# Optimization experiments

Hardware: AMD Instinct MI355X
Metric: run time of the kernel (lower is better)

Reference implementation:

```python
import jax, jax.numpy as jnp
import numpy as np

B, T, E, H = 4, 2048, 1024, 2048  # note: T must equal H (mask shape constraint in source)


def setup_inputs() -> dict:
    key = jax.random.key(0)
    ks = jax.random.split(key, 5)
    x = jax.random.normal(ks[0], (B, T, E), dtype=jnp.float32)
    Wq = jax.random.normal(ks[1], (E, H), dtype=jnp.float32) * 0.02
    bq = jnp.zeros((H,), dtype=jnp.float32)
    Wv = jax.random.normal(ks[2], (E, H), dtype=jnp.float32) * 0.02
    bv = jnp.zeros((H,), dtype=jnp.float32)
    return {"x": x, "Wq": Wq, "bq": bq, "Wv": Wv, "bv": bv}


def reference(x, Wq, bq, Wv, bv):
    # NOTE: original code uses q_proj for BOTH q and k (k = self.q_proj(x)),
    # so k is identical to q; k_proj params are dead. We reproduce that.
    q = x @ Wq + bq                                  # [B, T, H]
    v = x @ Wv + bv                                  # [B, T, H]
    scores = jnp.einsum('bqd,bkd->bqk', q, q)        # q @ k.mT with k == q
    scaled = scores / jnp.sqrt(jnp.float32(Wq.shape[1]))
    mask = jnp.tril(jnp.ones((scaled.shape[1], scaled.shape[2]), dtype=scaled.dtype))
    masked = scaled * mask                           # multiplicative mask (as in source)
    attn = jax.nn.softmax(masked, axis=1)            # softmax over dim=1 (query axis), as in source
    return attn @ v                                  # [B, T, H]
```

## Files before the change

kernel.cpp:

```cpp
#include <hip/hip_runtime.h>


#define B_DIM 4
#define T_DIM 2048
#define E_DIM 1024
#define H_DIM 2048

typedef __attribute__((ext_vector_type(8))) short bf16x8;
typedef __attribute__((ext_vector_type(4))) short s16x4;
typedef __attribute__((ext_vector_type(4))) float f32x4;

__device__ __forceinline__ float bf2f(short s) {
  union { float f; unsigned u; } x; x.u = ((unsigned)(unsigned short)s) << 16; return x.f;
}
__device__ __forceinline__ short f2bf(float f) {
  union { float f; unsigned u; } x; x.f = f;
  unsigned r = x.u + 0x7fff + ((x.u >> 16) & 1);
  return (short)(r >> 16);
}

__device__ __forceinline__ void gload16(const short* g, short* l) {
  __builtin_amdgcn_global_load_lds(
      (const __attribute__((address_space(1))) void*)g,
      (__attribute__((address_space(3))) void*)l, 16, 0, 0);
}

__device__ __forceinline__ void bar() {
  __builtin_amdgcn_sched_barrier(0);
  __builtin_amdgcn_s_barrier();
  __builtin_amdgcn_sched_barrier(0);
}

__global__ __launch_bounds__(512, 2) void gemm_pv(
    const short* __restrict__ Pg, const short* __restrict__ Vg,
    float* __restrict__ Cg, const float* __restrict__ sfx)
{
  __shared__ __align__(16) short lds[24576];

  const int t = threadIdx.x;
  const int lane = t & 63, wave = t >> 6;
  const int wm = wave >> 2, wn = wave & 3;
  const int l16 = lane & 15, kg = lane >> 4;

  const int lin = blockIdx.x + 256 * blockIdx.y;
  const int rt = 15 - (lin >> 5);
  const int rem = lin & 31;
  const int ct = rem >> 2, bz = rem & 3;

  const int K = T_DIM, N = H_DIM;
  const short* A  = Pg + (long)bz * T_DIM * T_DIM + (long)rt * 128 * K;
  const short* Bv = Vg + (long)bz * H_DIM * T_DIM + (long)ct * 256 * K;
  const int NT = (rt + 1) * 2;

  const int fA = t >> 3, cA = (t & 7) ^ (fA & 7);
  const long sA0 = (long)(2 * fA + (cA >> 2)) * K + (cA & 3) * 8;
  const int dA0 = t * 8;
  long sB[2]; int dB[2];
#pragma unroll
  for (int j = 0; j < 2; ++j) {
    const int cid = j * 512 + t;
    const int f = cid >> 3, c = (cid & 7) ^ (f & 7);
    sB[j] = (long)(2 * f + (c >> 2)) * K + (c & 3) * 8;
    dB[j] = cid * 8;
  }

  const int fl = l16 >> 1;
  const int slot = (((l16 & 1) * 4 + kg) ^ fl) & 7;
  const int abase = (wm * 32 + fl) * 64 + slot * 8;
  const int bbase = 8192 + (wn * 32 + fl) * 64 + slot * 8;

  f32x4 acc[4][4] = {};

  for (int tt = 0; tt < NT; ++tt) {
    const long k0 = (long)tt * 64;
    __syncthreads();
    gload16(A  + sA0   + k0,      &lds[dA0]);
    gload16(A  + sA0   + k0 + 32, &lds[4096 + dA0]);
    gload16(Bv + sB[0] + k0,      &lds[8192 + dB[0]]);
    gload16(Bv + sB[1] + k0,      &lds[8192 + dB[1]]);
    gload16(Bv + sB[0] + k0 + 32, &lds[16384 + dB[0]]);
    gload16(Bv + sB[1] + k0 + 32, &lds[16384 + dB[1]]);
    __syncthreads();
#pragma unroll
    for (int kk = 0; kk < 2; ++kk) {
      bf16x8 bfr[4];
#pragma unroll
      for (int ni = 0; ni < 4; ++ni)
        bfr[ni] = *(const bf16x8*)&lds[bbase + kk * 8192 + ni * 512];
#pragma unroll
      for (int mi = 0; mi < 4; ++mi) {
        const bf16x8 a = *(const bf16x8*)&lds[abase + kk * 4096 + mi * 512];
#pragma unroll
        for (int ni = 0; ni < 4; ++ni)
          acc[mi][ni] = __builtin_amdgcn_mfma_f32_16x16x32_bf16(a, bfr[ni], acc[mi][ni], 0, 0, 0);
      }
    }
  }

  float* C = Cg + (long)bz * T_DIM * H_DIM;
  const float* sf = sfx + ((long)bz * 16 + rt) * N;
  const int rowb = rt * 128 + wm * 64 + kg * 4;
  const int colb = ct * 256 + wn * 64 + l16;
#pragma unroll
  for (int mi = 0; mi < 4; ++mi)
#pragma unroll
    for (int ni = 0; ni < 4; ++ni) {
      const int col = colb + ni * 16;
      const float s = sf[col];
#pragma unroll
      for (int r = 0; r < 4; ++r)
        C[(long)(rowb + mi * 16 + r) * N + col] = acc[mi][ni][r] + s;
    }
}

template<int MODE>
__global__ __launch_bounds__(512, 2) void gemm256(
    const short* __restrict__ Ag, const short* __restrict__ Bg,
    const float* __restrict__ bias, const float* __restrict__ bias2,
    void* __restrict__ Cg, void* __restrict__ Cg2,
    const float* __restrict__ sfx,
    int N, int K, long sA, long sB, long sC)
{
  __shared__ __align__(16) short lds[2 * 32768];

  const int t = threadIdx.x;
  const int lane = t & 63, wave = t >> 6;
  const int wm = wave >> 2, wn = wave & 3;
  const int l16 = lane & 15, kg = lane >> 4;

  int rt, ct, bz;
  {
    int lin = blockIdx.y * gridDim.x + blockIdx.x;
    const int cpx = (gridDim.x * gridDim.y) >> 3;
    lin = (lin & 7) * cpx + (lin >> 3);
    rt = lin / gridDim.x; ct = lin - rt * gridDim.x;
    bz = 0;
  }

  const short* A  = Ag + (long)bz * sA + (long)rt * 256 * K;
  const short* Bp = Bg + (long)bz * sB + (long)ct * 256 * K;
  const int kEnd = K;
  const int NT = kEnd >> 6;

  long soff[2];
  int dsto[2];
#pragma unroll
  for (int j = 0; j < 2; ++j) {
    const int cid = j * 512 + t;
    const int f = cid >> 3, sl = cid & 7;
    const int c = sl ^ (f & 7);
    soff[j] = (long)(2 * f + (c >> 2)) * K + (c & 3) * 8;
    dsto[j] = cid * 8;
  }

  const int fl = l16 >> 1;
  const int slot = (((l16 & 1) * 4 + kg) ^ fl) & 7;
  const int aoff = (wm * 64 + fl) * 64 + slot * 8;
  const int boff = (wn * 32 + fl) * 64 + slot * 8;

  f32x4 acc[8][4] = {};

  {
    short* S = lds;
#pragma unroll
    for (int kh = 0; kh < 2; ++kh)
#pragma unroll
      for (int j = 0; j < 2; ++j) {
        gload16(A  + soff[j] + kh * 32, &S[kh * 8192 + dsto[j]]);
        gload16(Bp + soff[j] + kh * 32, &S[16384 + kh * 8192 + dsto[j]]);
      }
  }
  asm volatile("s_waitcnt vmcnt(4)");
  __builtin_amdgcn_sched_barrier(0);
  bar();

  for (int T = 0; T < NT; ++T) {
    const short* Abase = lds + (T & 1) * 32768;
    short* S = lds + ((T + 1) & 1) * 32768;
    const long kIss = (long)(T + 1) * 64;
    const bool st = (T + 1) < NT;
    bf16x8 bfr[4], af[4];

    {
      const short* Ab = Abase;
      const short* Bb = Abase + 16384;
#pragma unroll
      for (int n = 0; n < 4; ++n) bfr[n] = *(const bf16x8*)&Bb[boff + n * 512];
#pragma unroll
      for (int m = 0; m < 4; ++m) af[m] = *(const bf16x8*)&Ab[aoff + m * 512];
      if (st) {
        gload16(A + soff[0] + kIss, &S[dsto[0]]);
        gload16(A + soff[1] + kIss, &S[dsto[1]]);
      }
      bar();
      __builtin_amdgcn_s_setprio(1);
#pragma unroll
      for (int m = 0; m < 4; ++m)
#pragma unroll
        for (int n = 0; n < 4; ++n)
          acc[m][n] = __builtin_amdgcn_mfma_f32_16x16x32_bf16(af[m], bfr[n], acc[m][n], 0, 0, 0);
      __builtin_amdgcn_s_setprio(0);
      bar();
    }
    {
      const short* Ab = Abase;
#pragma unroll
      for (int m = 0; m < 4; ++m) af[m] = *(const bf16x8*)&Ab[aoff + (m + 4) * 512];
      if (st) {
        gload16(Bp + soff[0] + kIss, &S[16384 + dsto[0]]);
        gload16(Bp + soff[1] + kIss, &S[16384 + dsto[1]]);
      }
      bar();
      __builtin_amdgcn_s_setprio(1);
#pragma unroll
      for (int m = 0; m < 4; ++m)
#pragma unroll
        for (int n = 0; n < 4; ++n)
          acc[m + 4][n] = __builtin_amdgcn_mfma_f32_16x16x32_bf16(af[m], bfr[n], acc[m + 4][n], 0, 0, 0);
      __builtin_amdgcn_s_setprio(0);
      if (T == NT - 1) asm volatile("s_waitcnt vmcnt(0)");
      else             asm volatile("s_waitcnt vmcnt(4)");
      __builtin_amdgcn_sched_barrier(0);
      bar();
    }
    {
      const short* Ab = Abase + 8192;
      const short* Bb = Abase + 16384 + 8192;
#pragma unroll
      for (int n = 0; n < 4; ++n) bfr[n] = *(const bf16x8*)&Bb[boff + n * 512];
#pragma unroll
      for (int m = 0; m < 4; ++m) af[m] = *(const bf16x8*)&Ab[aoff + m * 512];
      if (st) {
        gload16(A + soff[0] + kIss + 32, &S[8192 + dsto[0]]);
        gload16(A + soff[1] + kIss + 32, &S[8192 + dsto[1]]);
      }
      bar();
      __builtin_amdgcn_s_setprio(1);
#pragma unroll
      for (int m = 0; m < 4; ++m)
#pragma unroll
        for (int n = 0; n < 4; ++n)
          acc[m][n] = __builtin_amdgcn_mfma_f32_16x16x32_bf16(af[m], bfr[n], acc[m][n], 0, 0, 0);
      __builtin_amdgcn_s_setprio(0);
      bar();
    }
    {
      const short* Ab = Abase + 8192;
#pragma unroll
      for (int m = 0; m < 4; ++m) af[m] = *(const bf16x8*)&Ab[aoff + (m + 4) * 512];
      if (st) {
        gload16(Bp + soff[0] + kIss + 32, &S[16384 + 8192 + dsto[0]]);
        gload16(Bp + soff[1] + kIss + 32, &S[16384 + 8192 + dsto[1]]);
      }
      bar();
      __builtin_amdgcn_s_setprio(1);
#pragma unroll
      for (int m = 0; m < 4; ++m)
#pragma unroll
        for (int n = 0; n < 4; ++n)
          acc[m + 4][n] = __builtin_amdgcn_mfma_f32_16x16x32_bf16(af[m], bfr[n], acc[m + 4][n], 0, 0, 0);
      __builtin_amdgcn_s_setprio(0);
      if (st) {
        asm volatile("s_waitcnt vmcnt(4)");
        __builtin_amdgcn_sched_barrier(0);
      }
      bar();
    }
  }

  __syncthreads();

  {
    short* Cs = lds;
    const int Nh = N >> 1;
#pragma unroll
    for (int m = 0; m < 8; ++m)
#pragma unroll
      for (int n = 0; n < 4; ++n) {
        const int cl = wn * 64 + n * 16 + l16;
        const int colg = ct * 256 + cl;
        const float bv = (colg < Nh) ? bias[colg] : bias2[colg - Nh];
#pragma unroll
        for (int r = 0; r < 4; ++r) {
          const int rl = wm * 128 + m * 16 + kg * 4 + r;
          *(short*)((char*)Cs + (((((rl << 8) + cl) << 1)) ^ ((rl & 7) << 4))) =
              f2bf(acc[m][n][r] + bv);
        }
      }
    __syncthreads();
    short* C = ((ct * 256) < Nh) ? (short*)Cg : (short*)Cg2;
    const int rr = t >> 1, hc = (t & 1) * 128;
    const long gbase = (long)(rt * 256 + rr) * Nh + ((ct * 256) & (Nh - 1)) + hc;
#pragma unroll
    for (int j = 0; j < 16; ++j)
      *(bf16x8*)(C + gbase + j * 8) =
          *(const bf16x8*)((const char*)Cs +
              ((((rr << 8) + hc + (j << 3)) << 1) ^ ((rr & 7) << 4)));
  }
}

template<int MODE>
__global__ __launch_bounds__(256) void gemm_bt(
    const short* __restrict__ Ag, const short* __restrict__ Bg,
    const float* __restrict__ bias, const float* __restrict__ bias2,
    void* __restrict__ Cg, void* __restrict__ Cg2,
    float* __restrict__ colsum, const float* __restrict__ sfx,
    int M, int N, int K, long sA, long sB, long sC, float scale)
{
  __shared__ __align__(16) short lds[128 * 64 * 2];
  short* As = lds;
  short* Bs = lds + 128 * 64;
  __shared__ float csum[128];

  const int t = threadIdx.x;
  const int bz = blockIdx.z;

  int rt, ct;
  {
    int idx = 135 - blockIdx.x;
    rt = (int)((sqrtf(8.0f * idx + 1.0f) - 1.0f) * 0.5f);
    while ((rt + 1) * (rt + 2) / 2 <= idx) rt++;
    while (rt * (rt + 1) / 2 > idx) rt--;
    ct = idx - rt * (rt + 1) / 2;
  }

  const short* A = Ag + (long)bz * sA + (long)rt * 128 * K;
  const short* B = Bg + (long)bz * sB + (long)ct * 128 * K;
  const int kEnd = K;

  const int lane = t & 63;
  const int wave = t >> 6;
  const int wr = wave >> 1, wc = wave & 1;
  const int l16 = lane & 15, kg = lane >> 4;

  if (t < 128) csum[t] = (rt == ct) ? 128.0f * ct : 0.0f;

  f32x4 acc[4][4] = {};

  for (int k0 = 0; k0 < kEnd; k0 += 64) {
    __syncthreads();
#pragma unroll
    for (int j = 0; j < 4; ++j) {
      const int e = j * 256 + t;
      const int r = e >> 3, cl = e & 7;
      const int cg = cl ^ (r & 7);
      gload16(A + (long)r * K + (k0 + cg * 8), &As[e * 8]);
      gload16(B + (long)r * K + (k0 + cg * 8), &Bs[e * 8]);
    }
    __syncthreads();
#pragma unroll
    for (int kk = 0; kk < 2; ++kk) {
      bf16x8 af[4], bfr[4];
#pragma unroll
      for (int mi = 0; mi < 4; ++mi)
        af[mi] = *(const bf16x8*)&As[(wr * 64 + mi * 16 + l16) * 64 +
                                     ((kk * 4 + kg) ^ (l16 & 7)) * 8];
#pragma unroll
      for (int ni = 0; ni < 4; ++ni)
        bfr[ni] = *(const bf16x8*)&Bs[(wc * 64 + ni * 16 + l16) * 64 +
                                      ((kk * 4 + kg) ^ (l16 & 7)) * 8];
#pragma unroll
      for (int mi = 0; mi < 4; ++mi)
#pragma unroll
        for (int ni = 0; ni < 4; ++ni)
          acc[mi][ni] = __builtin_amdgcn_mfma_f32_16x16x32_bf16(af[mi], bfr[ni], acc[mi][ni], 0, 0, 0);
    }
  }

  {
    short* Cs = lds;
    __syncthreads();
    float ps[4] = {0.f, 0.f, 0.f, 0.f};
#pragma unroll
    for (int mi = 0; mi < 4; ++mi)
#pragma unroll
      for (int ni = 0; ni < 4; ++ni) {
        const int cl = wc * 64 + ni * 16 + l16;
        const int col = ct * 128 + cl;
#pragma unroll
        for (int r = 0; r < 4; ++r) {
          const int rl = wr * 64 + kg * 4 + mi * 16 + r;
          const int row = rt * 128 + rl;
          float e = (row >= col) ? __expf(acc[mi][ni][r] * scale) : 1.0f;
          Cs[rl * 128 + cl] = f2bf(e);
          ps[ni] += e;
        }
      }
#pragma unroll
    for (int ni = 0; ni < 4; ++ni)
      atomicAdd(&csum[wc * 64 + ni * 16 + l16], ps[ni]);
    __syncthreads();
    short* C = (short*)Cg + (long)bz * sC;
    const int rr = t >> 1, cc = (t & 1) * 64;
    const long gbase = (long)(rt * 128 + rr) * N + ct * 128 + cc;
#pragma unroll
    for (int j = 0; j < 8; ++j)
      *(bf16x8*)(C + gbase + j * 8) = *(const bf16x8*)&Cs[rr * 128 + cc + j * 8];
    if (t < 128)
      atomicAdd(&colsum[(long)bz * N + ct * 128 + t], csum[t]);
  }
}

__global__ __launch_bounds__(256) void f32_to_bf16(
    const float* __restrict__ src, short* __restrict__ dst, long n)
{
  long i = ((long)blockIdx.x * blockDim.x + threadIdx.x) * 4;
  if (i < n) {
    const float4 v = *(const float4*)(src + i);
    s16x4 o;
    o.x = f2bf(v.x); o.y = f2bf(v.y); o.z = f2bf(v.z); o.w = f2bf(v.w);
    *(s16x4*)(dst + i) = o;
  }
}

__global__ __launch_bounds__(256) void wtrans(
    const float* __restrict__ src0, const float* __restrict__ src1,
    short* __restrict__ dst)
{
  __shared__ short tile[64][65];
  const int t = threadIdx.x;
  const int c0 = blockIdx.x * 64;
  const int r0 = blockIdx.y * 64;
  const float* s = blockIdx.z ? src1 : src0;
  short* d = dst + (long)blockIdx.z * H_DIM * E_DIM;
  const int rl = t >> 4, cb = (t & 15) * 4;
#pragma unroll
  for (int i = 0; i < 4; ++i) {
    int r = rl + i * 16;
    const float4 w = *(const float4*)(s + (long)(r0 + r) * H_DIM + c0 + cb);
    tile[r][cb + 0] = f2bf(w.x); tile[r][cb + 1] = f2bf(w.y);
    tile[r][cb + 2] = f2bf(w.z); tile[r][cb + 3] = f2bf(w.w);
  }
  __syncthreads();
#pragma unroll
  for (int i = 0; i < 4; ++i) {
    int rr = rl + i * 16;
    s16x4 o;
    o.x = tile[cb + 0][rr]; o.y = tile[cb + 1][rr];
    o.z = tile[cb + 2][rr]; o.w = tile[cb + 3][rr];
    *(s16x4*)(d + (long)(c0 + rr) * E_DIM + r0 + cb) = o;
  }
}

__global__ __launch_bounds__(256) void vtrans(
    const short* __restrict__ src, short* __restrict__ dst,
    const float* __restrict__ sums)
{
  __shared__ short tile[64][65];
  const int t = threadIdx.x;
  const int c0 = blockIdx.x * 64;
  const int r0 = blockIdx.y * 64;
  const int bz = blockIdx.z;
  const short* s = src + (long)bz * T_DIM * H_DIM;
  short* d = dst + (long)bz * H_DIM * T_DIM;
  const float* su = sums + (long)bz * T_DIM;
  const int rl = t >> 4, cb = (t & 15) * 4;
#pragma unroll
  for (int i = 0; i < 4; ++i) {
    int r = rl + i * 16;
    const float rs = 1.0f / su[r0 + r];
    const s16x4 w = *(const s16x4*)(s + (long)(r0 + r) * H_DIM + c0 + cb);
    tile[r][cb + 0] = f2bf(bf2f(w.x) * rs); tile[r][cb + 1] = f2bf(bf2f(w.y) * rs);
    tile[r][cb + 2] = f2bf(bf2f(w.z) * rs); tile[r][cb + 3] = f2bf(bf2f(w.w) * rs);
  }
  __syncthreads();
#pragma unroll
  for (int i = 0; i < 4; ++i) {
    int rr = rl + i * 16;
    s16x4 o;
    o.x = tile[cb + 0][rr]; o.y = tile[cb + 1][rr];
    o.z = tile[cb + 2][rr]; o.w = tile[cb + 3][rr];
    *(s16x4*)(d + (long)(c0 + rr) * T_DIM + r0 + cb) = o;
  }
}

__global__ __launch_bounds__(256) void block_psum(
    const short* __restrict__ v, const float* __restrict__ colsum,
    float* __restrict__ psum)
{
  const int h = (blockIdx.x * 256 + threadIdx.x) * 2;
  const int j = blockIdx.y, bz = blockIdx.z;
  const short* vb = v + (long)bz * T_DIM * H_DIM;
  const float* cs = colsum + (long)bz * T_DIM;
  float s0 = 0.f, s1 = 0.f;
  const int k0 = j * 128;
  for (int k = k0; k < k0 + 128; ++k) {
    union { int i; short s[2]; } w;
    w.i = *(const int*)(vb + (long)k * H_DIM + h);
    const float rs = 1.0f / cs[k];
    s0 += bf2f(w.s[0]) * rs;
    s1 += bf2f(w.s[1]) * rs;
  }
  float* p = psum + ((long)bz * 16 + j) * H_DIM + h;
  p[0] = s0; p[1] = s1;
}

__global__ __launch_bounds__(256) void suffix_scan(
    const float* __restrict__ psum, float* __restrict__ sfx)
{
  const int h = blockIdx.x * 256 + threadIdx.x;
  const int bz = blockIdx.z;
  const long base = (long)bz * 16 * H_DIM + h;
  float suf = 0.f;
  sfx[base + 15L * H_DIM] = 0.f;
  for (int j = 15; j >= 1; --j) {
    suf += psum[base + (long)j * H_DIM];
    sfx[base + (long)(j - 1) * H_DIM] = suf;
  }
}

extern "C" void kernel_launch(void* const* d_in, const int* in_sizes, int n_in,
                              void* d_out, int out_size, void* d_ws, size_t ws_size,
                              hipStream_t stream) {
  const float* x  = (const float*)d_in[0];
  const float* Wq = (const float*)d_in[1];
  const float* bq = (const float*)d_in[2];
  const float* Wv = (const float*)d_in[3];
  const float* bv = (const float*)d_in[4];
  float* out = (float*)d_out;

  char* ws = (char*)d_ws;
  short* P      = (short*)(ws);
  short* q      = (short*)(ws + (size_t)32 * 1024 * 1024);
  short* v      = (short*)(ws + (size_t)64 * 1024 * 1024);
  float* colsum = (float*)(ws + (size_t)96 * 1024 * 1024);
  float* sfx    = (float*)(ws + (size_t)96 * 1024 * 1024 + 32 * 1024);
  short* vT = q;

  short* xb    = (short*)d_out;
  short* WqvT  = (short*)((char*)d_out + (size_t)16 * 1024 * 1024);
  float* psum  = (float*)((char*)d_out + (size_t)24 * 1024 * 1024);

  const float scale = 0.022097086912079612f;
  dim3 blk(256);

  hipMemsetAsync(colsum, 0, (size_t)B_DIM * T_DIM * 4, stream);

  f32_to_bf16<<<dim3((B_DIM * T_DIM * E_DIM) / (256 * 4)), blk, 0, stream>>>(
      x, xb, (long)B_DIM * T_DIM * E_DIM);
  wtrans<<<dim3(H_DIM / 64, E_DIM / 64, 2), blk, 0, stream>>>(Wq, Wv, WqvT);

  gemm256<0><<<dim3((2 * H_DIM) / 256, (B_DIM * T_DIM) / 256, 1), dim3(512), 0, stream>>>(
      xb, WqvT, bq, bv, q, v, nullptr, 2 * H_DIM, E_DIM, 0, 0, 0);

  gemm_bt<1><<<dim3(136, 1, B_DIM), blk, 0, stream>>>(
      q, q, nullptr, nullptr, P, nullptr, colsum, nullptr, T_DIM, T_DIM, H_DIM,
      (long)T_DIM * H_DIM, (long)T_DIM * H_DIM, (long)T_DIM * T_DIM, scale);

  vtrans<<<dim3(H_DIM / 64, T_DIM / 64, B_DIM), blk, 0, stream>>>(v, vT, colsum);
  block_psum<<<dim3(H_DIM / 512, 16, B_DIM), blk, 0, stream>>>(v, colsum, psum);
  suffix_scan<<<dim3(H_DIM / 256, 1, B_DIM), blk, 0, stream>>>(psum, sfx);

  gemm_pv<<<dim3(256, 2, 1), dim3(512), 0, stream>>>(P, vT, out, sfx);
}
```

Before: 343.1 us.

## Fuse prep kernels, fold block psum into vtrans, inline suffix sum

Combines the memset, x-to-bf16 conversion and weight transpose into one prep launch. Block column partial sums are now accumulated inside vtrans through shared memory and global atomics, which removes the separate block_psum pass that re-read v. The suffix scan kernel is dropped and gemm_pv sums the remaining row-block partials itself in its epilogue. This cuts four launches and one full read of v, at the cost of atomics and a short serial loop in the epilogue.

Measured after the change: 338.2 us. About the same (-1.4%).

```diff
diff --git a/kernel.cpp b/kernel.cpp
--- a/kernel.cpp
+++ b/kernel.cpp
@@ -31,9 +31,56 @@
   __builtin_amdgcn_sched_barrier(0);
 }
 
+#define NCONV 8192
+__global__ __launch_bounds__(256) void prep(
+    const float* __restrict__ x, short* __restrict__ xb,
+    const float* __restrict__ Wq, const float* __restrict__ Wv,
+    short* __restrict__ WqvT, float* __restrict__ colsum,
+    float* __restrict__ psum)
+{
+  __shared__ short tile[64][65];
+  const int b = blockIdx.x;
+  const int t = threadIdx.x;
+  if (b < NCONV) {
+    const long tid = (long)b * 256 + t;
+    const long i = tid * 4;
+    const float4 v = *(const float4*)(x + i);
+    s16x4 o;
+    o.x = f2bf(v.x); o.y = f2bf(v.y); o.z = f2bf(v.z); o.w = f2bf(v.w);
+    *(s16x4*)(xb + i) = o;
+    if (tid < B_DIM * T_DIM) colsum[tid] = 0.f;
+    if (tid < (long)B_DIM * 16 * H_DIM) psum[tid] = 0.f;
+  } else {
+    int id = b - NCONV;
+    const int z = id >> 9;
+    id &= 511;
+    const int c0 = (id & 31) * 64;
+    const int r0 = (id >> 5) * 64;
+    const float* s = z ? Wv : Wq;
+    short* d = WqvT + (long)z * H_DIM * E_DIM;
+    const int rl = t >> 4, cb = (t & 15) * 4;
+#pragma unroll
+    for (int i = 0; i < 4; ++i) {
+      int r = rl + i * 16;
+      const float4 w = *(const float4*)(s + (long)(r0 + r) * H_DIM + c0 + cb);
+      tile[r][cb + 0] = f2bf(w.x); tile[r][cb + 1] = f2bf(w.y);
+      tile[r][cb + 2] = f2bf(w.z); tile[r][cb + 3] = f2bf(w.w);
+    }
+    __syncthreads();
+#pragma unroll
+    for (int i = 0; i < 4; ++i) {
+      int rr = rl + i * 16;
+      s16x4 o;
+      o.x = tile[cb + 0][rr]; o.y = tile[cb + 1][rr];
+      o.z = tile[cb + 2][rr]; o.w = tile[cb + 3][rr];
+      *(s16x4*)(d + (long)(c0 + rr) * E_DIM + r0 + cb) = o;
+    }
+  }
+}
+
 __global__ __launch_bounds__(512, 2) void gemm_pv(
     const short* __restrict__ Pg, const short* __restrict__ Vg,
-    float* __restrict__ Cg, const float* __restrict__ sfx)
+    float* __restrict__ Cg, const float* __restrict__ psum)
 {
   __shared__ __align__(16) short lds[24576];
 
@@ -98,7 +145,7 @@
   }
 
   float* C = Cg + (long)bz * T_DIM * H_DIM;
-  const float* sf = sfx + ((long)bz * 16 + rt) * N;
+  const float* ps = psum + (long)bz * 16 * N;
   const int rowb = rt * 128 + wm * 64 + kg * 4;
   const int colb = ct * 256 + wn * 64 + l16;
 #pragma unroll
@@ -106,7 +153,9 @@
 #pragma unroll
     for (int ni = 0; ni < 4; ++ni) {
       const int col = colb + ni * 16;
-      const float s = sf[col];
+      float s = 0.f;
+      for (int j = rt + 1; j < 16; ++j)
+        s += ps[(long)j * N + col];
 #pragma unroll
       for (int r = 0; r < 4; ++r)
         C[(long)(rowb + mi * 16 + r) * N + col] = acc[mi][ni][r] + s;
@@ -118,8 +167,7 @@
     const short* __restrict__ Ag, const short* __restrict__ Bg,
     const float* __restrict__ bias, const float* __restrict__ bias2,
     void* __restrict__ Cg, void* __restrict__ Cg2,
-    const float* __restrict__ sfx,
-    int N, int K, long sA, long sB, long sC)
+    int N, int K, long sA, long sB)
 {
   __shared__ __align__(16) short lds[2 * 32768];
 
@@ -128,19 +176,17 @@
   const int wm = wave >> 2, wn = wave & 3;
   const int l16 = lane & 15, kg = lane >> 4;
 
-  int rt, ct, bz;
+  int rt, ct;
   {
     int lin = blockIdx.y * gridDim.x + blockIdx.x;
     const int cpx = (gridDim.x * gridDim.y) >> 3;
     lin = (lin & 7) * cpx + (lin >> 3);
     rt = lin / gridDim.x; ct = lin - rt * gridDim.x;
-    bz = 0;
-  }
-
-  const short* A  = Ag + (long)bz * sA + (long)rt * 256 * K;
-  const short* Bp = Bg + (long)bz * sB + (long)ct * 256 * K;
-  const int kEnd = K;
-  const int NT = kEnd >> 6;
+  }
+
+  const short* A  = Ag + (long)rt * 256 * K;
+  const short* Bp = Bg + (long)ct * 256 * K;
+  const int NT = K >> 6;
 
   long soff[2];
   int dsto[2];
@@ -299,13 +345,9 @@
   }
 }
 
-template<int MODE>
-__global__ __launch_bounds__(256) void gemm_bt(
-    const short* __restrict__ Ag, const short* __restrict__ Bg,
-    const float* __restrict__ bias, const float* __restrict__ bias2,
-    void* __restrict__ Cg, void* __restrict__ Cg2,
-    float* __restrict__ colsum, const float* __restrict__ sfx,
-    int M, int N, int K, long sA, long sB, long sC, float scale)
+__global__ __launch_bounds__(256) void gemm_sc(
+    const short* __restrict__ Ag, short* __restrict__ Cg,
+    float* __restrict__ colsum, int K, float scale)
 {
   __shared__ __align__(16) short lds[128 * 64 * 2];
   short* As = lds;
@@ -314,6 +356,7 @@
 
   const int t = threadIdx.x;
   const int bz = blockIdx.z;
+  const int M = T_DIM, N = T_DIM;
 
   int rt, ct;
   {
@@ -324,9 +367,8 @@
     ct = idx - rt * (rt + 1) / 2;
   }
 
-  const short* A = Ag + (long)bz * sA + (long)rt * 128 * K;
-  const short* B = Bg + (long)bz * sB + (long)ct * 128 * K;
-  const int kEnd = K;
+  const short* A = Ag + (long)bz * T_DIM * H_DIM + (long)rt * 128 * K;
+  const short* B = Ag + (long)bz * T_DIM * H_DIM + (long)ct * 128 * K;
 
   const int lane = t & 63;
   const int wave = t >> 6;
@@ -337,7 +379,7 @@
 
   f32x4 acc[4][4] = {};
 
-  for (int k0 = 0; k0 < kEnd; k0 += 64) {
+  for (int k0 = 0; k0 < K; k0 += 64) {
     __syncthreads();
 #pragma unroll
     for (int j = 0; j < 4; ++j) {
@@ -390,7 +432,7 @@
     for (int ni = 0; ni < 4; ++ni)
       atomicAdd(&csum[wc * 64 + ni * 16 + l16], ps[ni]);
     __syncthreads();
-    short* C = (short*)Cg + (long)bz * sC;
+    short* C = Cg + (long)bz * T_DIM * T_DIM;
     const int rr = t >> 1, cc = (t & 1) * 64;
     const long gbase = (long)(rt * 128 + rr) * N + ct * 128 + cc;
 #pragma unroll
@@ -401,52 +443,12 @@
   }
 }
 
-__global__ __launch_bounds__(256) void f32_to_bf16(
-    const float* __restrict__ src, short* __restrict__ dst, long n)
-{
-  long i = ((long)blockIdx.x * blockDim.x + threadIdx.x) * 4;
-  if (i < n) {
-    const float4 v = *(const float4*)(src + i);
-    s16x4 o;
-    o.x = f2bf(v.x); o.y = f2bf(v.y); o.z = f2bf(v.z); o.w = f2bf(v.w);
-    *(s16x4*)(dst + i) = o;
-  }
-}
-
-__global__ __launch_bounds__(256) void wtrans(
-    const float* __restrict__ src0, const float* __restrict__ src1,
-    short* __restrict__ dst)
+__global__ __launch_bounds__(256) void vtrans(
+    const short* __restrict__ src, short* __restrict__ dst,
+    const float* __restrict__ sums, float* __restrict__ psum)
 {
   __shared__ short tile[64][65];
-  const int t = threadIdx.x;
-  const int c0 = blockIdx.x * 64;
-  const int r0 = blockIdx.y * 64;
-  const float* s = blockIdx.z ? src1 : src0;
-  short* d = dst + (long)blockIdx.z * H_DIM * E_DIM;
-  const int rl = t >> 4, cb = (t & 15) * 4;
-#pragma unroll
-  for (int i = 0; i < 4; ++i) {
-    int r = rl + i * 16;
-    const float4 w = *(const float4*)(s + (long)(r0 + r) * H_DIM + c0 + cb);
-    tile[r][cb + 0] = f2bf(w.x); tile[r][cb + 1] = f2bf(w.y);
-    tile[r][cb + 2] = f2bf(w.z); tile[r][cb + 3] = f2bf(w.w);
-  }
-  __syncthreads();
-#pragma unroll
-  for (int i = 0; i < 4; ++i) {
-    int rr = rl + i * 16;
-    s16x4 o;
-    o.x = tile[cb + 0][rr]; o.y = tile[cb + 1][rr];
-    o.z = tile[cb + 2][rr]; o.w = tile[cb + 3][rr];
-    *(s16x4*)(d + (long)(c0 + rr) * E_DIM + r0 + cb) = o;
-  }
-}
-
-__global__ __launch_bounds__(256) void vtrans(
-    const short* __restrict__ src, short* __restrict__ dst,
-    const float* __restrict__ sums)
-{
-  __shared__ short tile[64][65];
+  __shared__ float cacc[64];
   const int t = threadIdx.x;
   const int c0 = blockIdx.x * 64;
   const int r0 = blockIdx.y * 64;
@@ -455,15 +457,22 @@
   short* d = dst + (long)bz * H_DIM * T_DIM;
   const float* su = sums + (long)bz * T_DIM;
   const int rl = t >> 4, cb = (t & 15) * 4;
+  if (t < 64) cacc[t] = 0.f;
+  float p4[4] = {0.f, 0.f, 0.f, 0.f};
 #pragma unroll
   for (int i = 0; i < 4; ++i) {
     int r = rl + i * 16;
     const float rs = 1.0f / su[r0 + r];
     const s16x4 w = *(const s16x4*)(s + (long)(r0 + r) * H_DIM + c0 + cb);
-    tile[r][cb + 0] = f2bf(bf2f(w.x) * rs); tile[r][cb + 1] = f2bf(bf2f(w.y) * rs);
-    tile[r][cb + 2] = f2bf(bf2f(w.z) * rs); tile[r][cb + 3] = f2bf(bf2f(w.w) * rs);
+    const float f0 = bf2f(w.x) * rs, f1 = bf2f(w.y) * rs;
+    const float f2 = bf2f(w.z) * rs, f3 = bf2f(w.w) * rs;
+    tile[r][cb + 0] = f2bf(f0); tile[r][cb + 1] = f2bf(f1);
+    tile[r][cb + 2] = f2bf(f2); tile[r][cb + 3] = f2bf(f3);
+    p4[0] += f0; p4[1] += f1; p4[2] += f2; p4[3] += f3;
   }
   __syncthreads();
+#pragma unroll
+  for (int j = 0; j < 4; ++j) atomicAdd(&cacc[cb + j], p4[j]);
 #pragma unroll
   for (int i = 0; i < 4; ++i) {
     int rr = rl + i * 16;
@@ -472,41 +481,9 @@
     o.z = tile[cb + 2][rr]; o.w = tile[cb + 3][rr];
     *(s16x4*)(d + (long)(c0 + rr) * T_DIM + r0 + cb) = o;
   }
-}
-
-__global__ __launch_bounds__(256) void block_psum(
-    const short* __restrict__ v, const float* __restrict__ colsum,
-    float* __restrict__ psum)
-{
-  const int h = (blockIdx.x * 256 + threadIdx.x) * 2;
-  const int j = blockIdx.y, bz = blockIdx.z;
-  const short* vb = v + (long)bz * T_DIM * H_DIM;
-  const float* cs = colsum + (long)bz * T_DIM;
-  float s0 = 0.f, s1 = 0.f;
-  const int k0 = j * 128;
-  for (int k = k0; k < k0 + 128; ++k) {
-    union { int i; short s[2]; } w;
-    w.i = *(const int*)(vb + (long)k * H_DIM + h);
-    const float rs = 1.0f / cs[k];
-    s0 += bf2f(w.s[0]) * rs;
-    s1 += bf2f(w.s[1]) * rs;
-  }
-  float* p = psum + ((long)bz * 16 + j) * H_DIM + h;
-  p[0] = s0; p[1] = s1;
-}
-
-__global__ __launch_bounds__(256) void suffix_scan(
-    const float* __restrict__ psum, float* __restrict__ sfx)
-{
-  const int h = blockIdx.x * 256 + threadIdx.x;
-  const int bz = blockIdx.z;
-  const long base = (long)bz * 16 * H_DIM + h;
-  float suf = 0.f;
-  sfx[base + 15L * H_DIM] = 0.f;
-  for (int j = 15; j >= 1; --j) {
-    suf += psum[base + (long)j * H_DIM];
-    sfx[base + (long)(j - 1) * H_DIM] = suf;
-  }
+  __syncthreads();
+  if (t < 64)
+    atomicAdd(&psum[((long)bz * 16 + (r0 >> 7)) * H_DIM + c0 + t], cacc[t]);
 }
 
 extern "C" void kernel_launch(void* const* d_in, const int* in_sizes, int n_in,
@@ -524,32 +501,25 @@
   short* q      = (short*)(ws + (size_t)32 * 1024 * 1024);
   short* v      = (short*)(ws + (size_t)64 * 1024 * 1024);
   float* colsum = (float*)(ws + (size_t)96 * 1024 * 1024);
-  float* sfx    = (float*)(ws + (size_t)96 * 1024 * 1024 + 32 * 1024);
+  float* psum   = (float*)(ws + (size_t)96 * 1024 * 1024 + 32 * 1024);
   short* vT = q;
 
   short* xb    = (short*)d_out;
   short* WqvT  = (short*)((char*)d_out + (size_t)16 * 1024 * 1024);
-  float* psum  = (float*)((char*)d_out + (size_t)24 * 1024 * 1024);
 
   const float scale = 0.022097086912079612f;
-  dim3 blk(256);
-
-  hipMemsetAsync(colsum, 0, (size_t)B_DIM * T_DIM * 4, stream);
-
-  f32_to_bf16<<<dim3((B_DIM * T_DIM * E_DIM) / (256 * 4)), blk, 0, stream>>>(
-      x, xb, (long)B_DIM * T_DIM * E_DIM);
-  wtrans<<<dim3(H_DIM / 64, E_DIM / 64, 2), blk, 0, stream>>>(Wq, Wv, WqvT);
+
+  prep<<<dim3(NCONV + 1024), dim3(256), 0, stream>>>(
+      x, xb, Wq, Wv, WqvT, colsum, psum);
 
   gemm256<0><<<dim3((2 * H_DIM) / 256, (B_DIM * T_DIM) / 256, 1), dim3(512), 0, stream>>>(
-      xb, WqvT, bq, bv, q, v, nullptr, 2 * H_DIM, E_DIM, 0, 0, 0);
-
-  gemm_bt<1><<<dim3(136, 1, B_DIM), blk, 0, stream>>>(
-      q, q, nullptr, nullptr, P, nullptr, colsum, nullptr, T_DIM, T_DIM, H_DIM,
-      (long)T_DIM * H_DIM, (long)T_DIM * H_DIM, (long)T_DIM * T_DIM, scale);
-
-  vtrans<<<dim3(H_DIM / 64, T_DIM / 64, B_DIM), blk, 0, stream>>>(v, vT, colsum);
-  block_psum<<<dim3(H_DIM / 512, 16, B_DIM), blk, 0, stream>>>(v, colsum, psum);
-  suffix_scan<<<dim3(H_DIM / 256, 1, B_DIM), blk, 0, stream>>>(psum, sfx);
-
-  gemm_pv<<<dim3(256, 2, 1), dim3(512), 0, stream>>>(P, vT, out, sfx);
-}
+      xb, WqvT, bq, bv, q, v, 2 * H_DIM, E_DIM, 0, 0);
+
+  gemm_sc<<<dim3(136, 1, B_DIM), dim3(256), 0, stream>>>(
+      q, P, colsum, H_DIM, scale);
+
+  vtrans<<<dim3(H_DIM / 64, T_DIM / 64, B_DIM), dim3(256), 0, stream>>>(
+      v, vT, colsum, psum);
+
+  gemm_pv<<<dim3(256, 2, 1), dim3(512), 0, stream>>>(P, vT, out, psum);
+}
```
